# Optimization experiments

Hardware: AMD Instinct MI355X
Metric: run time of the kernel (lower is better)

The kernel has to match this reference:

```python
import jax, jax.numpy as jnp
import numpy as np

N, E, NG, H, BD, L, B = 4000, 50000, 12, 128, 128, 2, 100

def _gelu(x):
    return jax.nn.gelu(x, approximate=False)

def forward(pos, vel, charges, grid0, rand_SO3, batch, edge_index,
            W_basis1, b_basis1, W_basis2, b_basis2,
            W_fbasis1, b_fbasis1, W_fbasis2, b_fbasis2,
            W_embed, W_conv, W_fiber, b_conv, ln_gamma, ln_beta,
            W_ff1, b_ff1, W_ff2, b_ff2, W_ro1, b_ro1, W_ro2, b_ro2):
    n_nodes = pos.shape[0]
    n_graphs = rand_SO3.shape[0]
    n = grid0.shape[0]
    src, dst = edge_index[0], edge_index[1]
    # per-graph randomly rotated S2 grid
    grid_graph = jnp.einsum('bij,nj->bni', rand_SO3, grid0)    # [B,n,3]
    grid_node = grid_graph[batch]                               # [N,n,3]
    grid_edge = grid_node[src]                                  # [E,n,3]
    # R3S2 Euclidean invariants (separable): parallel + perpendicular parts of rel_pos wrt each grid orientation
    rel = pos[src] - pos[dst]                                   # [E,3]
    inv1 = jnp.einsum('ed,end->en', rel, grid_edge)[..., None]  # [E,n,1]
    inv2 = jnp.linalg.norm(rel[:, None, :] - inv1 * grid_edge, axis=-1, keepdims=True)
    cp = (charges[src] * charges[dst])[:, None, :]              # [E,1,1]
    ei = jnp.concatenate([inv1, inv2, jnp.broadcast_to(cp, inv1.shape)], -1)  # [E,n,3]
    # PolynomialFeatures(degree=2): [x, flatten(x outer x)] -> 3+9=12
    ei_poly = jnp.concatenate([ei, (ei[..., :, None] * ei[..., None, :]).reshape(ei.shape[:-1] + (9,))], -1)
    basis = _gelu(_gelu(ei_poly @ W_basis1 + b_basis1) @ W_basis2 + b_basis2)  # [E,n,BD]
    # fiber invariants: pairwise grid dot products (rotation cancels) -> [n,n,1]; poly deg 2 -> [n,n,2]
    fi = jnp.sum(grid0[:, None, :] * grid0[None, :, :], -1, keepdims=True)
    fi_poly = jnp.concatenate([fi, fi * fi], -1)
    fiber_basis = _gelu(_gelu(fi_poly @ W_fbasis1 + b_fbasis1) @ W_fbasis2 + b_fbasis2)  # [n,n,BD]
    # node features projected to sphere
    ones = jnp.ones((n_nodes, 1), pos.dtype)
    cnt = jax.ops.segment_sum(ones, batch, num_segments=n_graphs)
    mean_pos = jax.ops.segment_sum(pos, batch, num_segments=n_graphs) / jnp.maximum(cnt, 1.0)
    rel_pos = pos - mean_pos[batch]
    v_sph = jnp.einsum('nd,nkd->nk', vel, grid_node)[..., None]
    p_sph = jnp.einsum('nd,nkd->nk', rel_pos, grid_node)[..., None]
    c_sph = jnp.broadcast_to(charges[:, None, :], (n_nodes, n, 1))
    vn = jnp.linalg.norm(vel, axis=-1, keepdims=True)
    vn_sph = jnp.broadcast_to(vn[:, None, :], (n_nodes, n, 1))
    x = jnp.concatenate([v_sph, p_sph, c_sph, vn_sph], -1) @ W_embed  # [N,n,H]
    # SeparableBundleConvNext stack
    for l in range(W_conv.shape[0]):
        kern = basis @ W_conv[l]                                       # [E,n,H]
        x1 = jax.ops.segment_sum(x[src] * kern, dst, num_segments=n_nodes)  # depthwise spatial conv + scatter-add
        fk = fiber_basis @ W_fiber[l]                                  # [n,n,H]
        x2 = jnp.einsum('boc,poc->bpc', x1, fk) / n + b_conv[l]        # depthwise fiber conv
        mu = jnp.mean(x2, -1, keepdims=True)
        var = jnp.mean((x2 - mu) ** 2, -1, keepdims=True)
        h = (x2 - mu) / jnp.sqrt(var + 1e-5) * ln_gamma[l] + ln_beta[l]
        h = _gelu(h @ W_ff1[l] + b_ff1[l]) @ W_ff2[l] + b_ff2[l]
        x = x + h
    y = _gelu(x @ W_ro1 + b_ro1) @ W_ro2 + b_ro2                       # [N,n,1]
    return jnp.mean(grid_node * y, axis=-2)                            # sphere2vec -> [N,3]

def setup_inputs():
    key = jax.random.key(0)
    ks = jax.random.split(key, 24)
    f = jnp.float32
    # deterministic uniform-ish S2 grid (fibonacci sphere)
    i = np.arange(NG) + 0.5
    phi = np.arccos(1.0 - 2.0 * i / NG)
    th = np.pi * (1.0 + 5.0 ** 0.5) * i
    grid0 = jnp.asarray(np.stack([np.sin(phi) * np.cos(th), np.sin(phi) * np.sin(th), np.cos(phi)], -1), f)
    # random SO(3) per graph via unit quaternions
    q = jax.random.normal(ks[0], (B, 4), f)
    q = q / jnp.linalg.norm(q, axis=-1, keepdims=True)
    w, xq, yq, zq = q[:, 0], q[:, 1], q[:, 2], q[:, 3]
    R = jnp.stack([
        jnp.stack([1 - 2 * (yq ** 2 + zq ** 2), 2 * (xq * yq - zq * w), 2 * (xq * zq + yq * w)], -1),
        jnp.stack([2 * (xq * yq + zq * w), 1 - 2 * (xq ** 2 + zq ** 2), 2 * (yq * zq - xq * w)], -1),
        jnp.stack([2 * (xq * zq - yq * w), 2 * (yq * zq + xq * w), 1 - 2 * (xq ** 2 + yq ** 2)], -1)], -2)
    s = 0.05
    return dict(
        pos=jax.random.normal(ks[1], (N, 3), f),
        vel=jax.random.normal(ks[2], (N, 3), f),
        charges=jax.random.normal(ks[3], (N, 1), f),
        batch=jnp.sort(jax.random.randint(ks[4], (N,), 0, B)),
        edge_index=jax.random.randint(ks[5], (2, E), 0, N),
        grid0=grid0, rand_SO3=R,
        W_basis1=jax.random.normal(ks[6], (12, H), f) * s, b_basis1=jnp.zeros((H,), f),
        W_basis2=jax.random.normal(ks[7], (H, BD), f) * s, b_basis2=jnp.zeros((BD,), f),
        W_fbasis1=jax.random.normal(ks[8], (2, H), f) * s, b_fbasis1=jnp.zeros((H,), f),
        W_fbasis2=jax.random.normal(ks[9], (H, BD), f) * s, b_fbasis2=jnp.zeros((BD,), f),
        W_embed=jax.random.normal(ks[10], (4, H), f) * s,
        W_conv=jax.random.normal(ks[11], (L, BD, H), f) * s,
        W_fiber=jax.random.normal(ks[12], (L, BD, H), f) * s,
        b_conv=jnp.zeros((L, H), f),
        ln_gamma=jnp.ones((L, H), f), ln_beta=jnp.zeros((L, H), f),
        W_ff1=jax.random.normal(ks[13], (L, H, 4 * H), f) * s, b_ff1=jnp.zeros((L, 4 * H), f),
        W_ff2=jax.random.normal(ks[14], (L, 4 * H, H), f) * s, b_ff2=jnp.zeros((L, H), f),
        W_ro1=jax.random.normal(ks[15], (H, H), f) * s, b_ro1=jnp.zeros((H,), f),
        W_ro2=jax.random.normal(ks[16], (H, 1), f) * s, b_ro2=jnp.zeros((1,), f),
    )

def reference(pos, vel, charges, batch, edge_index, grid0, rand_SO3,
              W_basis1, b_basis1, W_basis2, b_basis2,
              W_fbasis1, b_fbasis1, W_fbasis2, b_fbasis2,
              W_embed, W_conv, W_fiber, b_conv, ln_gamma, ln_beta,
              W_ff1, b_ff1, W_ff2, b_ff2, W_ro1, b_ro1, W_ro2, b_ro2):
    return forward(pos, vel, charges, grid0, rand_SO3, batch, edge_index,
                   W_basis1, b_basis1, W_basis2, b_basis2,
                   W_fbasis1, b_fbasis1, W_fbasis2, b_fbasis2,
                   W_embed, W_conv, W_fiber, b_conv, ln_gamma, ln_beta,
                   W_ff1, b_ff1, W_ff2, b_ff2, W_ro1, b_ro1, W_ro2, b_ro2)
```

## Files before the change

### kernel.cpp

```cpp
#include <hip/hip_runtime.h>

typedef unsigned short u16;
typedef short s16x8 __attribute__((ext_vector_type(8)));
typedef float f32x4 __attribute__((ext_vector_type(4)));

constexpr int NNODES = 4000;
constexpr int NEDGES = 50000;
constexpr int NGRID  = 12;
constexpr int HD     = 128;
constexpr int H4     = 512;
constexpr int NLAY   = 2;

constexpr size_t OFF_GN   = 0;
constexpr size_t OFF_PS   = 144000;
constexpr size_t OFF_CNT  = 144304;
constexpr size_t OFF_FK   = 144512;
constexpr size_t OFF_X    = 181376;
constexpr size_t OFF_X1   = 6325376;
constexpr size_t OFF_WB   = 12469376;
constexpr size_t OFF_ROWP = 12625024;
constexpr size_t OFF_DEG  = 12629032;
constexpr size_t OFF_CUR  = 12633032;
constexpr size_t OFF_ESRT = 12637032;
constexpr size_t OFF_EIPB = 12687032;
constexpr size_t OFF_W1T  = 17487416;
constexpr size_t OFF_SRCS = 17489464;
constexpr size_t OFF_END_SLOW = 17539464;
constexpr size_t OFF_BAS  = 17539464;
constexpr size_t KERN_F   = 38400000;
constexpr size_t OFF_END_FAST  = OFF_BAS + KERN_F;
constexpr size_t OFF_END_DUAL  = OFF_BAS + 2*KERN_F;

constexpr size_t WB_W2T = 0;
constexpr size_t WB_WCT = 16384;
constexpr size_t WB_F1T = 49152;
constexpr size_t WB_F2T = 180224;

__device__ __forceinline__ u16 f2bf(float f){
  union { float f; unsigned int i; } v; v.f = f;
  unsigned int x = v.i;
  x += 0x7fffu + ((x >> 16) & 1u);
  return (u16)(x >> 16);
}
__device__ __forceinline__ float bf2f(u16 u){
  union { unsigned int i; float f; } v; v.i = ((unsigned int)u) << 16; return v.f;
}
__device__ __forceinline__ float gelu_f(float x){
  return 0.5f * x * (1.0f + erff(x * 0.70710678118654752f));
}
__device__ __forceinline__ float waveReduceSum(float v){
  #pragma unroll
  for(int off = 32; off > 0; off >>= 1) v += __shfl_xor(v, off, 64);
  return v;
}
__device__ __forceinline__ f32x4 mfma16(s16x8 a, s16x8 b, f32x4 c){
  return __builtin_amdgcn_mfma_f32_16x16x32_bf16(a, b, c, 0, 0, 0);
}

__global__ void k_stats(const float* __restrict__ pos, const int* __restrict__ batch,
                        float* __restrict__ possum, float* __restrict__ pcnt){
  int n = blockIdx.x * 256 + threadIdx.x;
  if(n >= NNODES) return;
  int b = batch[n];
  atomicAdd(&possum[b*3+0], pos[n*3+0]);
  atomicAdd(&possum[b*3+1], pos[n*3+1]);
  atomicAdd(&possum[b*3+2], pos[n*3+2]);
  atomicAdd(&pcnt[b], 1.0f);
}

__global__ void k_gridnode(const float* __restrict__ g0, const float* __restrict__ R,
                           const int* __restrict__ batch, float* __restrict__ grid_node){
  int idx = blockIdx.x * 256 + threadIdx.x;
  if(idx >= NNODES*NGRID) return;
  int n = idx / NGRID, k = idx % NGRID;
  int b = batch[n];
  float g[3];
  #pragma unroll
  for(int j=0;j<3;j++) g[j] = g0[k*3+j];
  #pragma unroll
  for(int i=0;i<3;i++){
    float s = 0.f;
    #pragma unroll
    for(int j=0;j<3;j++) s += R[b*9+i*3+j] * g[j];
    grid_node[idx*3+i] = s;
  }
}

__global__ __launch_bounds__(128) void k_embed(
    const float* __restrict__ pos, const float* __restrict__ vel, const float* __restrict__ charges,
    const int* __restrict__ batch, const float* __restrict__ possum, const float* __restrict__ pcnt,
    const float* __restrict__ grid_node, const float* __restrict__ W_embed, float* __restrict__ x)
{
  int n = blockIdx.x; int t = threadIdx.x;
  __shared__ float feats[NGRID][4];
  __shared__ float sgn[NGRID][3];
  if(t < 36) sgn[t/3][t%3] = grid_node[n*36 + t];
  __syncthreads();
  if(t < NGRID){
    int b = batch[n];
    float inv = 1.0f / fmaxf(pcnt[b], 1.0f);
    float v0=vel[n*3], v1=vel[n*3+1], v2=vel[n*3+2];
    float p0=pos[n*3]   - possum[b*3]*inv;
    float p1=pos[n*3+1] - possum[b*3+1]*inv;
    float p2=pos[n*3+2] - possum[b*3+2]*inv;
    float g0=sgn[t][0], g1=sgn[t][1], g2=sgn[t][2];
    feats[t][0] = v0*g0 + v1*g1 + v2*g2;
    feats[t][1] = p0*g0 + p1*g1 + p2*g2;
    feats[t][2] = charges[n];
    feats[t][3] = sqrtf(v0*v0 + v1*v1 + v2*v2);
  }
  __syncthreads();
  float w0=W_embed[0*HD+t], w1=W_embed[1*HD+t];
  float w2=W_embed[2*HD+t], w3=W_embed[3*HD+t];
  #pragma unroll
  for(int k=0;k<NGRID;k++)
    x[(n*NGRID+k)*HD + t] = feats[k][0]*w0 + feats[k][1]*w1 + feats[k][2]*w2 + feats[k][3]*w3;
}

__global__ __launch_bounds__(128) void k_fiber(
    const float* __restrict__ g0, const float* __restrict__ Wf1, const float* __restrict__ bfb1,
    const float* __restrict__ Wf2, const float* __restrict__ bfb2, const float* __restrict__ W_fiber,
    float* __restrict__ fk)
{
  int po = blockIdx.x; int p = po / NGRID, o = po % NGRID; int c = threadIdx.x;
  __shared__ float st[HD];
  __shared__ float sfb[HD];
  float fi = 0.f;
  #pragma unroll
  for(int j=0;j<3;j++) fi += g0[p*3+j] * g0[o*3+j];
  float f2 = fi*fi;
  st[c] = gelu_f(fi*Wf1[c] + f2*Wf1[HD+c] + bfb1[c]);
  __syncthreads();
  float a = bfb2[c];
  for(int j=0;j<HD;j++) a += st[j] * Wf2[j*HD+c];
  sfb[c] = gelu_f(a);
  __syncthreads();
  for(int l=0;l<NLAY;l++){
    float s = 0.f;
    for(int j=0;j<HD;j++) s += sfb[j] * W_fiber[l*HD*HD + j*HD + c];
    fk[(l*144 + po)*HD + c] = s;
  }
}

__global__ void k_prep(const float* __restrict__ W_b2, const float* __restrict__ W_b1,
                       const float* __restrict__ W_conv, const float* __restrict__ W_ff1,
                       const float* __restrict__ W_ff2,
                       u16* __restrict__ W2T, u16* __restrict__ W1T, u16* __restrict__ WCT,
                       u16* __restrict__ F1T, u16* __restrict__ F2T){
  int idx = blockIdx.x * 256 + threadIdx.x;
  if(idx < 16384){
    int r = idx >> 7, c = idx & 127;
    W2T[c*128 + r] = f2bf(W_b2[idx]);
    return;
  }
  idx -= 16384;
  if(idx < 4096){
    int c = idx >> 5, f = idx & 31;
    W1T[idx] = (f < 12) ? f2bf(W_b1[f*HD + c]) : (u16)0;
    return;
  }
  idx -= 4096;
  if(idx < 32768){
    int l = idx >> 14, j = idx & 16383;
    int r = j >> 7, c = j & 127;
    WCT[l*16384 + c*128 + r] = f2bf(W_conv[l*16384 + j]);
    return;
  }
  idx -= 32768;
  if(idx < 131072){
    int l = idx >> 16, j = idx & 65535;
    int r = j / 512, c = j % 512;
    F1T[l*65536 + c*128 + r] = f2bf(W_ff1[l*65536 + j]);
    return;
  }
  idx -= 131072;
  if(idx < 131072){
    int l = idx >> 16, j = idx & 65535;
    int r = j / 128, c = j % 128;
    F2T[l*65536 + c*512 + r] = f2bf(W_ff2[l*65536 + j]);
  }
}

__global__ void k_prepro(const float* __restrict__ W_ro1, u16* __restrict__ RO1T){
  int idx = blockIdx.x * 256 + threadIdx.x;
  if(idx >= 16384) return;
  int r = idx >> 7, c = idx & 127;
  RO1T[c*128 + r] = f2bf(W_ro1[idx]);
}

__global__ void k_deg(const int* __restrict__ eidx, int* __restrict__ deg){
  int e = blockIdx.x * 256 + threadIdx.x;
  if(e >= NEDGES) return;
  atomicAdd(&deg[eidx[NEDGES + e]], 1);
}

__global__ __launch_bounds__(256) void k_scan(const int* __restrict__ deg, int* __restrict__ rowptr){
  int t = threadIdx.x;
  __shared__ int part[256];
  int base = t * 16;
  int lp[16]; int s = 0;
  #pragma unroll
  for(int i=0;i<16;i++){
    int idx = base + i;
    int v = (idx < NNODES) ? deg[idx] : 0;
    lp[i] = s; s += v;
  }
  part[t] = s;
  __syncthreads();
  for(int off=1; off<256; off<<=1){
    int v2 = (t >= off) ? part[t-off] : 0;
    __syncthreads();
    part[t] += v2;
    __syncthreads();
  }
  int excl = part[t] - s;
  #pragma unroll
  for(int i=0;i<16;i++){
    int idx = base + i;
    if(idx < NNODES) rowptr[idx] = excl + lp[i];
  }
  if(t == 255) rowptr[NNODES] = part[255];
}

__global__ void k_bucket(const int* __restrict__ eidx, const int* __restrict__ rowptr,
                         int* __restrict__ cur, int* __restrict__ esorted, int* __restrict__ srcs){
  int e = blockIdx.x * 256 + threadIdx.x;
  if(e >= NEDGES) return;
  int d = eidx[NEDGES + e];
  int p = atomicAdd(&cur[d], 1);
  int slot = rowptr[d] + p;
  esorted[slot] = e;
  srcs[slot] = eidx[e];
}

__global__ void k_einv(const int* __restrict__ esorted, const int* __restrict__ eidx,
                       const float* __restrict__ pos, const float* __restrict__ charges,
                       const float* __restrict__ grid_node, u16* __restrict__ eipb){
  int row = blockIdx.x * 256 + threadIdx.x;
  if(row >= NEDGES*NGRID) return;
  int p = row / NGRID, kg = row - p*NGRID;
  int e = esorted[p];
  int sr = eidx[e], ds = eidx[NEDGES + e];
  float r0 = pos[sr*3]   - pos[ds*3];
  float r1 = pos[sr*3+1] - pos[ds*3+1];
  float r2 = pos[sr*3+2] - pos[ds*3+2];
  float cp = charges[sr] * charges[ds];
  float g0 = grid_node[sr*36 + kg*3];
  float g1 = grid_node[sr*36 + kg*3 + 1];
  float g2 = grid_node[sr*36 + kg*3 + 2];
  float inv1 = r0*g0 + r1*g1 + r2*g2;
  float d0 = r0 - inv1*g0, d1 = r1 - inv1*g1, d2 = r2 - inv1*g2;
  float inv2 = sqrtf(d0*d0 + d1*d1 + d2*d2);
  float ei[3] = {inv1, inv2, cp};
  s16x8 lo, hi;
  #pragma unroll
  for(int i=0;i<3;i++) lo[i] = (short)f2bf(ei[i]);
  lo[3] = (short)f2bf(ei[0]*ei[0]);
  lo[4] = (short)f2bf(ei[0]*ei[1]);
  lo[5] = (short)f2bf(ei[0]*ei[2]);
  lo[6] = (short)f2bf(ei[1]*ei[0]);
  lo[7] = (short)f2bf(ei[1]*ei[1]);
  hi[0] = (short)f2bf(ei[1]*ei[2]);
  hi[1] = (short)f2bf(ei[2]*ei[0]);
  hi[2] = (short)f2bf(ei[2]*ei[1]);
  hi[3] = (short)f2bf(ei[2]*ei[2]);
  hi[4] = 0; hi[5] = 0; hi[6] = 0; hi[7] = 0;
  *(s16x8*)&eipb[(size_t)row*16]     = lo;
  *(s16x8*)&eipb[(size_t)row*16 + 8] = hi;
}

constexpr int T1S = 136;

__global__ __launch_bounds__(256) void k_kern(
    const u16* __restrict__ eipb, const u16* __restrict__ W1T,
    const float* __restrict__ b1, const float* __restrict__ b2,
    const u16* __restrict__ W2T, const u16* __restrict__ WCT,
    u16* __restrict__ kern, int nl, size_t kstride)
{
  int t = threadIdx.x;
  int lane = t & 63, w = t >> 6, quad = lane >> 4, l16 = lane & 15;
  size_t R0 = (size_t)blockIdx.x * 64;
  __shared__ __align__(16) u16 s_buf[64*T1S];

  float b1v[2], b2v[2];
  #pragma unroll
  for(int nt=0;nt<2;nt++){
    b1v[nt] = b1[(2*w+nt)*16 + l16];
    b2v[nt] = b2[(2*w+nt)*16 + l16];
  }
  const s16x8 zvec = {0,0,0,0,0,0,0,0};

  {
    f32x4 a1[4][2];
    #pragma unroll
    for(int mt=0;mt<4;mt++)
      #pragma unroll
      for(int nt=0;nt<2;nt++) a1[mt][nt] = (f32x4){0.f,0.f,0.f,0.f};
    s16x8 Af[4];
    #pragma unroll
    for(int mt=0;mt<4;mt++){
      s16x8 v = *(const s16x8*)&eipb[(R0 + mt*16 + l16)*16 + (quad&1)*8];
      if(quad >= 2) v = zvec;
      Af[mt] = v;
    }
    #pragma unroll
    for(int nt=0;nt<2;nt++){
      s16x8 Bf = *(const s16x8*)&W1T[((2*w+nt)*16 + l16)*32 + quad*8];
      #pragma unroll
      for(int mt=0;mt<4;mt++) a1[mt][nt] = mfma16(Af[mt], Bf, a1[mt][nt]);
    }
    #pragma unroll
    for(int mt=0;mt<4;mt++)
      #pragma unroll
      for(int nt=0;nt<2;nt++)
        #pragma unroll
        for(int i=0;i<4;i++)
          s_buf[(mt*16 + quad*4 + i)*T1S + (2*w+nt)*16 + l16] = f2bf(gelu_f(a1[mt][nt][i] + b1v[nt]));
  }
  __syncthreads();
  f32x4 a2[4][2];
  #pragma unroll
  for(int mt=0;mt<4;mt++)
    #pragma unroll
    for(int nt=0;nt<2;nt++) a2[mt][nt] = (f32x4){0.f,0.f,0.f,0.f};
  #pragma unroll
  for(int ks=0; ks<4; ks++){
    s16x8 Af[4];
    #pragma unroll
    for(int mt=0;mt<4;mt++)
      Af[mt] = *(const s16x8*)&s_buf[(mt*16 + l16)*T1S + ks*32 + quad*8];
    #pragma unroll
    for(int nt=0;nt<2;nt++){
      s16x8 Bf = *(const s16x8*)&W2T[((2*w+nt)*16 + l16)*HD + ks*32 + quad*8];
      #pragma unroll
      for(int mt=0;mt<4;mt++) a2[mt][nt] = mfma16(Af[mt], Bf, a2[mt][nt]);
    }
  }
  __syncthreads();
  #pragma unroll
  for(int mt=0;mt<4;mt++)
    #pragma unroll
    for(int nt=0;nt<2;nt++)
      #pragma unroll
      for(int i=0;i<4;i++)
        s_buf[(mt*16 + quad*4 + i)*T1S + (2*w+nt)*16 + l16] = f2bf(gelu_f(a2[mt][nt][i] + b2v[nt]));
  __syncthreads();
  for(int l=0; l<nl; l++){
    f32x4 a3[4][2];
    #pragma unroll
    for(int mt=0;mt<4;mt++)
      #pragma unroll
      for(int nt=0;nt<2;nt++) a3[mt][nt] = (f32x4){0.f,0.f,0.f,0.f};
    #pragma unroll
    for(int ks=0; ks<4; ks++){
      s16x8 Af[4];
      #pragma unroll
      for(int mt=0;mt<4;mt++)
        Af[mt] = *(const s16x8*)&s_buf[(mt*16 + l16)*T1S + ks*32 + quad*8];
      #pragma unroll
      for(int nt=0;nt<2;nt++){
        s16x8 Bf = *(const s16x8*)&WCT[l*16384 + ((2*w+nt)*16 + l16)*HD + ks*32 + quad*8];
        #pragma unroll
        for(int mt=0;mt<4;mt++) a3[mt][nt] = mfma16(Af[mt], Bf, a3[mt][nt]);
      }
    }
    #pragma unroll
    for(int mt=0;mt<4;mt++)
      #pragma unroll
      for(int nt=0;nt<2;nt++)
        #pragma unroll
        for(int i=0;i<4;i++)
          kern[l*kstride + (R0 + mt*16 + quad*4 + i)*HD + (2*w+nt)*16 + l16] = f2bf(a3[mt][nt][i]);
  }
}

__global__ __launch_bounds__(256) void k_gather(
    const u16* __restrict__ kern, const float* __restrict__ x,
    const int* __restrict__ rowptr, const int* __restrict__ srcs,
    const float* __restrict__ fkl, const float* __restrict__ bconv,
    const float* __restrict__ gamma, const float* __restrict__ beta,
    u16* __restrict__ hout)
{
  int n = blockIdx.x, t = threadIdx.x;
  int c = t & 127, half = t >> 7;
  int w = t >> 6, lane = t & 63;
  __shared__ float raw[NGRID*HD];
  __shared__ float red[4][6], red2[4][6];
  int base = rowptr[n];
  int d = rowptr[n+1] - base;
  float acc[6] = {0.f,0.f,0.f,0.f,0.f,0.f};
  int srcn = (d > 0) ? srcs[base] : 0;
  for(int e=0; e<d; e++){
    int nsrc = (e+1 < d) ? srcs[base+e+1] : 0;
    const u16*   kp = &kern[((size_t)(base+e)*NGRID + half*6)*HD + c];
    const float* xp = &x[((size_t)srcn*NGRID + half*6)*HD + c];
    #pragma unroll
    for(int kk=0;kk<6;kk++)
      acc[kk] += bf2f(kp[kk*HD]) * xp[kk*HD];
    srcn = nsrc;
  }
  #pragma unroll
  for(int kk=0;kk<6;kk++)
    raw[(half*6+kk)*HD + c] = acc[kk];
  __syncthreads();
  float bc = bconv[c];
  float v[6];
  #pragma unroll
  for(int kk=0;kk<6;kk++){
    int p = half*6 + kk;
    float a = 0.f;
    #pragma unroll
    for(int o=0;o<NGRID;o++)
      a += raw[o*HD + c] * fkl[(p*NGRID+o)*HD + c];
    v[kk] = a * (1.0f/12.0f) + bc;
  }
  #pragma unroll
  for(int kk=0;kk<6;kk++){
    float s = waveReduceSum(v[kk]);
    if(lane == 0) red[w][kk] = s;
  }
  __syncthreads();
  float dd[6];
  #pragma unroll
  for(int kk=0;kk<6;kk++){
    float mu = (red[half*2][kk] + red[half*2+1][kk]) * (1.0f/128.0f);
    dd[kk] = v[kk] - mu;
    float s2 = waveReduceSum(dd[kk]*dd[kk]);
    if(lane == 0) red2[w][kk] = s2;
  }
  __syncthreads();
  float ga = gamma[c], be = beta[c];
  #pragma unroll
  for(int kk=0;kk<6;kk++){
    float var = (red2[half*2][kk] + red2[half*2+1][kk]) * (1.0f/128.0f);
    float inv = 1.0f / sqrtf(var + 1e-5f);
    hout[((size_t)n*NGRID + half*6 + kk)*HD + c] = f2bf(dd[kk] * inv * ga + be);
  }
}

__global__ __launch_bounds__(256) void k_ff1(
    const u16* __restrict__ F1T, const float* __restrict__ bf1,
    const u16* __restrict__ hin, u16* __restrict__ h4)
{
  int t = threadIdx.x;
  size_t r0 = (size_t)blockIdx.x * 32;
  int lane = t & 63, w = t >> 6, quad = lane >> 4, l16 = lane & 15;
  __shared__ __align__(16) u16 sxh[32*T1S];
  for(int i=t; i<32*HD/8; i+=256){
    int r = (i*8) >> 7, cc = (i*8) & 127;
    *(s16x8*)&sxh[r*T1S + cc] = *(const s16x8*)&hin[r0*HD + (size_t)i*8];
  }
  __syncthreads();
  f32x4 acc[2][8];
  #pragma unroll
  for(int mt=0;mt<2;mt++)
    #pragma unroll
    for(int j=0;j<8;j++) acc[mt][j] = (f32x4){0.f,0.f,0.f,0.f};
  #pragma unroll
  for(int ks=0; ks<4; ks++){
    s16x8 Af0 = *(const s16x8*)&sxh[l16*T1S + ks*32 + quad*8];
    s16x8 Af1 = *(const s16x8*)&sxh[(16 + l16)*T1S + ks*32 + quad*8];
    #pragma unroll
    for(int j=0;j<8;j++){
      int nt = w*8 + j;
      s16x8 Bf = *(const s16x8*)&F1T[((size_t)(nt*16 + l16))*HD + ks*32 + quad*8];
      acc[0][j] = mfma16(Af0, Bf, acc[0][j]);
      acc[1][j] = mfma16(Af1, Bf, acc[1][j]);
    }
  }
  #pragma unroll
  for(int j=0;j<8;j++){
    int col = (w*8+j)*16 + l16;
    float bv = bf1[col];
    #pragma unroll
    for(int mt=0;mt<2;mt++)
      #pragma unroll
      for(int i=0;i<4;i++){
        int row = mt*16 + quad*4 + i;
        h4[(r0 + row)*H4 + col] = f2bf(gelu_f(acc[mt][j][i] + bv));
      }
  }
}

__global__ __launch_bounds__(256) void k_ff2(
    const u16* __restrict__ F2T, const float* __restrict__ bf2,
    const u16* __restrict__ h4, float* __restrict__ x)
{
  int t = threadIdx.x;
  size_t r0 = (size_t)blockIdx.x * 32;
  int lane = t & 63, w = t >> 6, quad = lane >> 4, l16 = lane & 15;
  f32x4 acc[2][2];
  #pragma unroll
  for(int mt=0;mt<2;mt++)
    #pragma unroll
    for(int j=0;j<2;j++) acc[mt][j] = (f32x4){0.f,0.f,0.f,0.f};
  for(int ks=0; ks<16; ks++){
    s16x8 Af0 = *(const s16x8*)&h4[(r0 + l16)*H4 + ks*32 + quad*8];
    s16x8 Af1 = *(const s16x8*)&h4[(r0 + 16 + l16)*H4 + ks*32 + quad*8];
    #pragma unroll
    for(int j=0;j<2;j++){
      int nt = w*2 + j;
      s16x8 Bf = *(const s16x8*)&F2T[((size_t)(nt*16 + l16))*H4 + ks*32 + quad*8];
      acc[0][j] = mfma16(Af0, Bf, acc[0][j]);
      acc[1][j] = mfma16(Af1, Bf, acc[1][j]);
    }
  }
  #pragma unroll
  for(int j=0;j<2;j++){
    int col = (w*2+j)*16 + l16;
    float bv = bf2[col];
    #pragma unroll
    for(int mt=0;mt<2;mt++)
      #pragma unroll
      for(int i=0;i<4;i++){
        size_t row = r0 + mt*16 + quad*4 + i;
        x[row*HD + col] += acc[mt][j][i] + bv;
      }
  }
}

__global__ __launch_bounds__(256) void k_conv_slow(
    const u16* __restrict__ eipb, const u16* __restrict__ W1T,
    const float* __restrict__ b1, const float* __restrict__ b2,
    const u16* __restrict__ W2T, const u16* __restrict__ WCT,
    const float* __restrict__ x,
    const int* __restrict__ rowptr, const int* __restrict__ srcs,
    float* __restrict__ x1o)
{
  int n = blockIdx.x; int t = threadIdx.x;
  int lane = t & 63, w = t >> 6, quad = lane >> 4, l16 = lane & 15;

  __shared__ __align__(16) u16 s_t1h[48*T1S];
  __shared__ __align__(16) u16 s_bas[48*T1S];
  __shared__ __align__(16) float accLDS[NGRID*HD];

  int base = rowptr[n];
  int d = rowptr[n+1] - base;

  float b1v[2], b2v[2];
  #pragma unroll
  for(int nt=0;nt<2;nt++){
    b1v[nt] = b1[(2*w+nt)*16 + l16];
    b2v[nt] = b2[(2*w+nt)*16 + l16];
  }

  for(int i=t; i<NGRID*HD; i+=256) accLDS[i] = 0.f;
  __syncthreads();

  f32x4 accv[3][2];
  #pragma unroll
  for(int mt=0;mt<3;mt++)
    #pragma unroll
    for(int nt=0;nt<2;nt++) accv[mt][nt] = (f32x4){0.f,0.f,0.f,0.f};

  const s16x8 zvec = {0,0,0,0,0,0,0,0};

  for(int ch=0; ch<d; ch+=4){
    size_t rowb = (size_t)(base + ch) * NGRID;
    s16x8 Af1[3];
    #pragma unroll
    for(int mt=0;mt<3;mt++){
      s16x8 v = *(const s16x8*)&eipb[(rowb + mt*16 + l16)*16 + (quad&1)*8];
      if(quad >= 2) v = zvec;
      Af1[mt] = v;
    }
    float xv[3][4][2];
    #pragma unroll
    for(int mt=0;mt<3;mt++)
      #pragma unroll
      for(int i=0;i<4;i++){
        int row = mt*16 + quad*4 + i;
        int e = row / 12;
        int k = row - e*12;
        int ei2 = base + ch + e;
        int srcn = srcs[min(ei2, NEDGES-1)];
        float m = (ch + e < d) ? 1.0f : 0.0f;
        const float* xp = &x[((size_t)srcn*NGRID + k)*HD + l16];
        #pragma unroll
        for(int nt=0;nt<2;nt++)
          xv[mt][i][nt] = xp[(2*w+nt)*16] * m;
      }
    {
      f32x4 a1[3][2];
      #pragma unroll
      for(int mt=0;mt<3;mt++)
        #pragma unroll
        for(int nt=0;nt<2;nt++) a1[mt][nt] = (f32x4){0.f,0.f,0.f,0.f};
      #pragma unroll
      for(int nt=0;nt<2;nt++){
        s16x8 Bf = *(const s16x8*)&W1T[((2*w+nt)*16 + l16)*32 + quad*8];
        #pragma unroll
        for(int mt=0;mt<3;mt++) a1[mt][nt] = mfma16(Af1[mt], Bf, a1[mt][nt]);
      }
      #pragma unroll
      for(int mt=0;mt<3;mt++)
        #pragma unroll
        for(int nt=0;nt<2;nt++)
          #pragma unroll
          for(int i=0;i<4;i++)
            s_t1h[(mt*16 + quad*4 + i)*T1S + (2*w+nt)*16 + l16] = f2bf(gelu_f(a1[mt][nt][i] + b1v[nt]));
    }
    __syncthreads();
    {
      f32x4 a2[3][2];
      #pragma unroll
      for(int mt=0;mt<3;mt++)
        #pragma unroll
        for(int nt=0;nt<2;nt++) a2[mt][nt] = (f32x4){0.f,0.f,0.f,0.f};
      #pragma unroll
      for(int ks=0; ks<4; ks++){
        s16x8 Af[3];
        #pragma unroll
        for(int mt=0;mt<3;mt++)
          Af[mt] = *(const s16x8*)&s_t1h[(mt*16 + l16)*T1S + ks*32 + quad*8];
        #pragma unroll
        for(int nt=0;nt<2;nt++){
          s16x8 Bf = *(const s16x8*)&W2T[((2*w+nt)*16 + l16)*HD + ks*32 + quad*8];
          #pragma unroll
          for(int mt=0;mt<3;mt++) a2[mt][nt] = mfma16(Af[mt], Bf, a2[mt][nt]);
        }
      }
      #pragma unroll
      for(int mt=0;mt<3;mt++)
        #pragma unroll
        for(int nt=0;nt<2;nt++)
          #pragma unroll
          for(int i=0;i<4;i++)
            s_bas[(mt*16 + quad*4 + i)*T1S + (2*w+nt)*16 + l16] = f2bf(gelu_f(a2[mt][nt][i] + b2v[nt]));
    }
    __syncthreads();
    {
      f32x4 a3[3][2];
      #pragma unroll
      for(int mt=0;mt<3;mt++)
        #pragma unroll
        for(int nt=0;nt<2;nt++) a3[mt][nt] = (f32x4){0.f,0.f,0.f,0.f};
      #pragma unroll
      for(int ks=0; ks<4; ks++){
        s16x8 Af[3];
        #pragma unroll
        for(int mt=0;mt<3;mt++)
          Af[mt] = *(const s16x8*)&s_bas[(mt*16 + l16)*T1S + ks*32 + quad*8];
        #pragma unroll
        for(int nt=0;nt<2;nt++){
          s16x8 Bf = *(const s16x8*)&WCT[((2*w+nt)*16 + l16)*HD + ks*32 + quad*8];
          #pragma unroll
          for(int mt=0;mt<3;mt++) a3[mt][nt] = mfma16(Af[mt], Bf, a3[mt][nt]);
        }
      }
      #pragma unroll
      for(int mt=0;mt<3;mt++)
        #pragma unroll
        for(int nt=0;nt<2;nt++)
          #pragma unroll
          for(int i=0;i<4;i++)
            accv[mt][nt][i] += a3[mt][nt][i] * xv[mt][i][nt];
    }
  }
  __syncthreads();
  #pragma unroll
  for(int mt=0;mt<3;mt++)
    #pragma unroll
    for(int nt=0;nt<2;nt++)
      #pragma unroll
      for(int i=0;i<4;i++){
        int row = mt*16 + quad*4 + i;
        int k = row % 12;
        atomicAdd(&accLDS[k*HD + (2*w+nt)*16 + l16], accv[mt][nt][i]);
      }
  __syncthreads();
  for(int i=t; i<NGRID*HD; i+=256)
    x1o[(size_t)n*NGRID*HD + i] = accLDS[i];
}

constexpr int STS = 520;
__global__ __launch_bounds__(256) void k_ffln(
    const u16* __restrict__ F1T, const float* __restrict__ bf1,
    const u16* __restrict__ F2T, const float* __restrict__ bf2,
    const float* __restrict__ x1raw,
    const float* __restrict__ fkl, const float* __restrict__ bconv,
    const float* __restrict__ gamma, const float* __restrict__ beta,
    float* __restrict__ x)
{
  int n = blockIdx.x; int t = threadIdx.x;
  int lane = t & 63, w = t >> 6, quad = lane >> 4, l16 = lane & 15;
  __shared__ __align__(16) float raw[NGRID*HD];
  __shared__ __align__(16) u16 sxh[16*T1S];
  __shared__ __align__(16) u16 st[16*STS];

  for(int i=t; i<NGRID*HD; i+=256) raw[i] = x1raw[(size_t)n*NGRID*HD + i];
  for(int i=t; i<4*T1S; i+=256) sxh[12*T1S + i] = 0;
  __syncthreads();

  {
    int c0 = lane, c1 = lane + 64;
    float bc0 = bconv[c0], bc1 = bconv[c1];
    float ga0 = gamma[c0], ga1 = gamma[c1];
    float be0 = beta[c0],  be1 = beta[c1];
    #pragma unroll
    for(int pp=0; pp<3; pp++){
      int p = w + pp*4;
      float a0 = 0.f, a1 = 0.f;
      #pragma unroll
      for(int o=0;o<NGRID;o++){
        a0 += raw[o*HD + c0] * fkl[(p*NGRID+o)*HD + c0];
        a1 += raw[o*HD + c1] * fkl[(p*NGRID+o)*HD + c1];
      }
      float v0 = a0 * (1.0f/12.0f) + bc0;
      float v1 = a1 * (1.0f/12.0f) + bc1;
      float mu = waveReduceSum(v0 + v1) * (1.0f/128.0f);
      float d0 = v0 - mu, d1 = v1 - mu;
      float var = waveReduceSum(d0*d0 + d1*d1) * (1.0f/128.0f);
      float inv = 1.0f / sqrtf(var + 1e-5f);
      sxh[p*T1S + c0] = f2bf(d0 * inv * ga0 + be0);
      sxh[p*T1S + c1] = f2bf(d1 * inv * ga1 + be1);
    }
  }
  __syncthreads();
  {
    f32x4 acc1[8];
    #pragma unroll
    for(int j=0;j<8;j++) acc1[j] = (f32x4){0.f,0.f,0.f,0.f};
    #pragma unroll
    for(int ks=0; ks<4; ks++){
      s16x8 Af = *(const s16x8*)&sxh[l16*T1S + ks*32 + quad*8];
      #pragma unroll
      for(int j=0;j<8;j++){
        int nt = w*8 + j;
        s16x8 Bf = *(const s16x8*)&F1T[((size_t)(nt*16 + l16))*HD + ks*32 + quad*8];
        acc1[j] = mfma16(Af, Bf, acc1[j]);
      }
    }
    #pragma unroll
    for(int j=0;j<8;j++){
      int col = (w*8+j)*16 + l16;
      float bv = bf1[col];
      #pragma unroll
      for(int i=0;i<4;i++){
        int row = quad*4 + i;
        st[row*STS + col] = f2bf(gelu_f(acc1[j][i] + bv));
      }
    }
  }
  __syncthreads();
  {
    f32x4 acc2[2];
    #pragma unroll
    for(int j=0;j<2;j++) acc2[j] = (f32x4){0.f,0.f,0.f,0.f};
    for(int ks=0; ks<16; ks++){
      s16x8 Af = *(const s16x8*)&st[l16*STS + ks*32 + quad*8];
      #pragma unroll
      for(int j=0;j<2;j++){
        int nt = w*2 + j;
        s16x8 Bf = *(const s16x8*)&F2T[((size_t)(nt*16 + l16))*H4 + ks*32 + quad*8];
        acc2[j] = mfma16(Af, Bf, acc2[j]);
      }
    }
    #pragma unroll
    for(int j=0;j<2;j++){
      int col = (w*2+j)*16 + l16;
      float bv = bf2[col];
      #pragma unroll
      for(int i=0;i<4;i++){
        int row = quad*4 + i;
        if(row < NGRID){
          size_t idx = ((size_t)n*NGRID + row)*HD + col;
          x[idx] += acc2[j][i] + bv;
        }
      }
    }
  }
}

__global__ __launch_bounds__(256) void k_readout(
    const float* __restrict__ x, const float* __restrict__ grid_node,
    const u16* __restrict__ RO1T, const float* __restrict__ br1,
    const float* __restrict__ Wr2, const float* __restrict__ br2,
    float* __restrict__ out)
{
  int t = threadIdx.x;
  int n0 = blockIdx.x * 2;
  int lane = t & 63, w = t >> 6, quad = lane >> 4, l16 = lane & 15;
  __shared__ __align__(16) u16 sxh[32*T1S];
  __shared__ float sy[32];
  if(t < 32) sy[t] = 0.f;
  for(int i=t; i<2*NGRID*HD; i+=256){
    int nd = i / (NGRID*HD), rem = i - nd*NGRID*HD;
    int r = rem >> 7, c = rem & 127;
    sxh[(nd*16 + r)*T1S + c] = f2bf(x[(size_t)n0*NGRID*HD + i]);
  }
  for(int i=t; i<4*T1S; i+=256){ sxh[12*T1S + i] = 0; sxh[28*T1S + i] = 0; }
  __syncthreads();
  f32x4 acc[2][2];
  #pragma unroll
  for(int mt=0;mt<2;mt++)
    #pragma unroll
    for(int j=0;j<2;j++) acc[mt][j] = (f32x4){0.f,0.f,0.f,0.f};
  #pragma unroll
  for(int ks=0; ks<4; ks++){
    s16x8 Af0 = *(const s16x8*)&sxh[l16*T1S + ks*32 + quad*8];
    s16x8 Af1 = *(const s16x8*)&sxh[(16 + l16)*T1S + ks*32 + quad*8];
    #pragma unroll
    for(int j=0;j<2;j++){
      int nt = w*2 + j;
      s16x8 Bf = *(const s16x8*)&RO1T[((size_t)(nt*16 + l16))*HD + ks*32 + quad*8];
      acc[0][j] = mfma16(Af0, Bf, acc[0][j]);
      acc[1][j] = mfma16(Af1, Bf, acc[1][j]);
    }
  }
  #pragma unroll
  for(int j=0;j<2;j++){
    int col = (w*2+j)*16 + l16;
    float bv = br1[col];
    float w2v = Wr2[col];
    #pragma unroll
    for(int mt=0;mt<2;mt++)
      #pragma unroll
      for(int i=0;i<4;i++){
        int row = quad*4 + i;
        if(row < NGRID)
          atomicAdd(&sy[mt*16 + row], gelu_f(acc[mt][j][i] + bv) * w2v);
      }
  }
  __syncthreads();
  if(t < 6){
    int nd = t / 3, d = t - nd*3;
    float b2v = br2[0];
    float s = 0.f;
    #pragma unroll
    for(int k=0;k<NGRID;k++)
      s += grid_node[((size_t)(n0+nd)*NGRID + k)*3 + d] * (sy[nd*16 + k] + b2v);
    out[(n0+nd)*3 + d] = s * (1.0f/12.0f);
  }
}

extern "C" void kernel_launch(void* const* d_in, const int* in_sizes, int n_in,
                              void* d_out, int out_size, void* d_ws, size_t ws_size,
                              hipStream_t stream)
{
  const float* pos      = (const float*)d_in[0];
  const float* vel      = (const float*)d_in[1];
  const float* charges  = (const float*)d_in[2];
  const int*   batch    = (const int*)d_in[3];
  const int*   eidx     = (const int*)d_in[4];
  const float* grid0    = (const float*)d_in[5];
  const float* R        = (const float*)d_in[6];
  const float* W_b1     = (const float*)d_in[7];
  const float* b_b1     = (const float*)d_in[8];
  const float* W_b2     = (const float*)d_in[9];
  const float* b_b2     = (const float*)d_in[10];
  const float* W_fb1    = (const float*)d_in[11];
  const float* b_fb1    = (const float*)d_in[12];
  const float* W_fb2    = (const float*)d_in[13];
  const float* b_fb2    = (const float*)d_in[14];
  const float* W_embed  = (const float*)d_in[15];
  const float* W_conv   = (const float*)d_in[16];
  const float* W_fiber  = (const float*)d_in[17];
  const float* b_conv   = (const float*)d_in[18];
  const float* ln_g     = (const float*)d_in[19];
  const float* ln_b     = (const float*)d_in[20];
  const float* W_ff1    = (const float*)d_in[21];
  const float* b_ff1    = (const float*)d_in[22];
  const float* W_ff2    = (const float*)d_in[23];
  const float* b_ff2    = (const float*)d_in[24];
  const float* W_ro1    = (const float*)d_in[25];
  const float* b_ro1    = (const float*)d_in[26];
  const float* W_ro2    = (const float*)d_in[27];
  const float* b_ro2    = (const float*)d_in[28];

  float* ws        = (float*)d_ws;
  float* grid_node = ws + OFF_GN;
  float* possum    = ws + OFF_PS;
  float* pcnt      = ws + OFF_CNT;
  float* fk        = ws + OFF_FK;
  float* x         = ws + OFF_X;
  float* x1        = ws + OFF_X1;
  u16*   WB        = (u16*)(ws + OFF_WB);
  u16*   W2T       = WB + WB_W2T;
  u16*   WCT       = WB + WB_WCT;
  u16*   F1T       = WB + WB_F1T;
  u16*   F2T       = WB + WB_F2T;
  int*   rowptr    = (int*)(ws + OFF_ROWP);
  int*   deg       = (int*)(ws + OFF_DEG);
  int*   cur       = (int*)(ws + OFF_CUR);
  int*   esorted   = (int*)(ws + OFF_ESRT);
  u16*   eipb      = (u16*)(ws + OFF_EIPB);
  u16*   W1T       = (u16*)(ws + OFF_W1T);
  int*   srcs      = (int*)(ws + OFF_SRCS);
  u16*   kern1     = (u16*)(ws + OFF_BAS);
  u16*   RO1T      = (u16*)(ws + OFF_ESRT);
  u16*   hbuf      = (u16*)x1;
  const size_t KSTR = (size_t)600000 * HD;

  const bool fast = (ws_size >= OFF_END_FAST * sizeof(float));
  const bool dual = (ws_size >= OFF_END_DUAL * sizeof(float));

  hipMemsetAsync(possum, 0, 512*sizeof(float), stream);
  hipMemsetAsync(deg, 0, NNODES*sizeof(int), stream);
  hipMemsetAsync(cur, 0, NNODES*sizeof(int), stream);
  hipMemsetAsync(eipb + (size_t)NEDGES*NGRID*16, 0, 48*16*sizeof(u16), stream);

  k_stats<<<(NNODES+255)/256, 256, 0, stream>>>(pos, batch, possum, pcnt);
  k_gridnode<<<(NNODES*NGRID+255)/256, 256, 0, stream>>>(grid0, R, batch, grid_node);
  k_embed<<<NNODES, 128, 0, stream>>>(pos, vel, charges, batch, possum, pcnt, grid_node, W_embed, x);
  k_fiber<<<144, 128, 0, stream>>>(grid0, W_fb1, b_fb1, W_fb2, b_fb2, W_fiber, fk);

  k_prep<<<(315392+255)/256, 256, 0, stream>>>(W_b2, W_b1, W_conv, W_ff1, W_ff2,
                                               W2T, W1T, WCT, F1T, F2T);

  k_deg<<<(NEDGES+255)/256, 256, 0, stream>>>(eidx, deg);
  k_scan<<<1, 256, 0, stream>>>(deg, rowptr);
  k_bucket<<<(NEDGES+255)/256, 256, 0, stream>>>(eidx, rowptr, cur, esorted, srcs);

  k_einv<<<(NEDGES*NGRID+255)/256, 256, 0, stream>>>(esorted, eidx, pos, charges, grid_node, eipb);
  k_prepro<<<64, 256, 0, stream>>>(W_ro1, RO1T);

  if(fast){
    if(dual)
      k_kern<<<9375, 256, 0, stream>>>(eipb, W1T, b_b1, b_b2, W2T, WCT, kern1, 2, KSTR);
    for(int l=0; l<NLAY; l++){
      if(!dual)
        k_kern<<<9375, 256, 0, stream>>>(eipb, W1T, b_b1, b_b2, W2T, WCT + (size_t)l*16384,
                                         kern1, 1, 0);
      const u16* kl = dual ? (kern1 + (size_t)l*KSTR) : kern1;
      u16* h4 = dual ? (kern1 + (size_t)l*KSTR) : kern1;
      k_gather<<<NNODES, 256, 0, stream>>>(kl, x, rowptr, srcs,
          fk + (size_t)l*144*HD, b_conv + l*HD, ln_g + l*HD, ln_b + l*HD, hbuf);
      k_ff1<<<NNODES*NGRID/32, 256, 0, stream>>>(F1T + (size_t)l*65536, b_ff1 + l*H4, hbuf, h4);
      k_ff2<<<NNODES*NGRID/32, 256, 0, stream>>>(F2T + (size_t)l*65536, b_ff2 + l*HD, h4, x);
    }
  } else {
    for(int l=0; l<NLAY; l++){
      k_conv_slow<<<NNODES, 256, 0, stream>>>(eipb, W1T, b_b1, b_b2, W2T, WCT + (size_t)l*16384,
          x, rowptr, srcs, x1);
      k_ffln<<<NNODES, 256, 0, stream>>>(F1T + (size_t)l*65536, b_ff1 + l*H4,
          F2T + (size_t)l*65536, b_ff2 + l*HD, x1,
          fk + (size_t)l*144*HD, b_conv + l*HD, ln_g + l*HD, ln_b + l*HD, x);
    }
  }

  k_readout<<<NNODES/2, 256, 0, stream>>>(x, grid_node, RO1T, b_ro1, W_ro2, b_ro2, (float*)d_out);
}
```

Before: 799.9 us.

## Process two nodes per block in gather with paired-channel vector loads and per-wave LayerNorm

The gather kernel now handles two destination nodes per 256-thread block, with each thread accumulating two adjacent channels through 32-bit bf16 and float2 loads. The per-grid-point LayerNorm is remapped so one wave owns a whole 128-channel row, which replaces the shared-memory cross-wave reductions and two of the barriers with plain wave reductions. This aims to cut memory instruction count and synchronisation in the edge gather. Per-node parallelism in the gather phase is halved. Two adjacent memsets (deg and cur) are merged into one call, which assumes the two buffers are contiguous in the workspace.

```diff
diff --git a/kernel.cpp b/kernel.cpp
--- a/kernel.cpp
+++ b/kernel.cpp
@@ -381,60 +381,68 @@
     const float* __restrict__ gamma, const float* __restrict__ beta,
     u16* __restrict__ hout)
 {
-  int n = blockIdx.x, t = threadIdx.x;
-  int c = t & 127, half = t >> 7;
-  int w = t >> 6, lane = t & 63;
-  __shared__ float raw[NGRID*HD];
-  __shared__ float red[4][6], red2[4][6];
-  int base = rowptr[n];
-  int d = rowptr[n+1] - base;
-  float acc[6] = {0.f,0.f,0.f,0.f,0.f,0.f};
-  int srcn = (d > 0) ? srcs[base] : 0;
-  for(int e=0; e<d; e++){
-    int nsrc = (e+1 < d) ? srcs[base+e+1] : 0;
-    const u16*   kp = &kern[((size_t)(base+e)*NGRID + half*6)*HD + c];
-    const float* xp = &x[((size_t)srcn*NGRID + half*6)*HD + c];
+  int t = threadIdx.x;
+  __shared__ float raw[2][NGRID*HD];
+  {
+    int nd = t >> 7;
+    int tt = t & 127;
+    int g  = tt >> 6;
+    int c2 = (tt & 63) * 2;
+    int n = blockIdx.x * 2 + nd;
+    int base = rowptr[n];
+    int d = rowptr[n+1] - base;
+    float2 acc[6];
+    #pragma unroll
+    for(int kk=0;kk<6;kk++){ acc[kk].x = 0.f; acc[kk].y = 0.f; }
+    int srcn = (d > 0) ? srcs[base] : 0;
+    for(int e=0; e<d; e++){
+      int nsrc = (e+1 < d) ? srcs[base+e+1] : 0;
+      const u16*   kp = &kern[((size_t)(base+e)*NGRID + g*6)*HD + c2];
+      const float* xp = &x[((size_t)srcn*NGRID + g*6)*HD + c2];
+      #pragma unroll
+      for(int kk=0;kk<6;kk++){
+        unsigned int u = *(const unsigned int*)(kp + kk*HD);
+        float2 xv = *(const float2*)(xp + kk*HD);
+        acc[kk].x += bf2f((u16)(u & 0xffffu)) * xv.x;
+        acc[kk].y += bf2f((u16)(u >> 16))     * xv.y;
+      }
+      srcn = nsrc;
+    }
     #pragma unroll
     for(int kk=0;kk<6;kk++)
-      acc[kk] += bf2f(kp[kk*HD]) * xp[kk*HD];
-    srcn = nsrc;
-  }
-  #pragma unroll
-  for(int kk=0;kk<6;kk++)
-    raw[(half*6+kk)*HD + c] = acc[kk];
-  __syncthreads();
-  float bc = bconv[c];
-  float v[6];
-  #pragma unroll
-  for(int kk=0;kk<6;kk++){
-    int p = half*6 + kk;
-    float a = 0.f;
-    #pragma unroll
-    for(int o=0;o<NGRID;o++)
-      a += raw[o*HD + c] * fkl[(p*NGRID+o)*HD + c];
-    v[kk] = a * (1.0f/12.0f) + bc;
-  }
-  #pragma unroll
-  for(int kk=0;kk<6;kk++){
-    float s = waveReduceSum(v[kk]);
-    if(lane == 0) red[w][kk] = s;
-  }
-  __syncthreads();
-  float dd[6];
-  #pragma unroll
-  for(int kk=0;kk<6;kk++){
-    float mu = (red[half*2][kk] + red[half*2+1][kk]) * (1.0f/128.0f);
-    dd[kk] = v[kk] - mu;
-    float s2 = waveReduceSum(dd[kk]*dd[kk]);
-    if(lane == 0) red2[w][kk] = s2;
-  }
-  __syncthreads();
-  float ga = gamma[c], be = beta[c];
-  #pragma unroll
-  for(int kk=0;kk<6;kk++){
-    float var = (red2[half*2][kk] + red2[half*2+1][kk]) * (1.0f/128.0f);
-    float inv = 1.0f / sqrtf(var + 1e-5f);
-    hout[((size_t)n*NGRID + half*6 + kk)*HD + c] = f2bf(dd[kk] * inv * ga + be);
+      *(float2*)&raw[nd][(g*6+kk)*HD + c2] = acc[kk];
+  }
+  __syncthreads();
+  {
+    int w = t >> 6, lane = t & 63;
+    int ndw = w >> 1, ph = w & 1;
+    int c2 = lane * 2;
+    int nn = blockIdx.x * 2 + ndw;
+    float2 bc = *(const float2*)&bconv[c2];
+    float2 ga = *(const float2*)&gamma[c2];
+    float2 be = *(const float2*)&beta[c2];
+    #pragma unroll
+    for(int kk=0;kk<6;kk++){
+      int p = ph*6 + kk;
+      float ax = 0.f, ay = 0.f;
+      #pragma unroll
+      for(int o=0;o<NGRID;o++){
+        float2 fv = *(const float2*)&fkl[(p*NGRID+o)*HD + c2];
+        float2 rv = *(const float2*)&raw[ndw][o*HD + c2];
+        ax += rv.x * fv.x;
+        ay += rv.y * fv.y;
+      }
+      float vx = ax * (1.0f/12.0f) + bc.x;
+      float vy = ay * (1.0f/12.0f) + bc.y;
+      float mu = waveReduceSum(vx + vy) * (1.0f/128.0f);
+      float dx = vx - mu, dy = vy - mu;
+      float var = waveReduceSum(dx*dx + dy*dy) * (1.0f/128.0f);
+      float inv = 1.0f / sqrtf(var + 1e-5f);
+      u16 h0 = f2bf(dx * inv * ga.x + be.x);
+      u16 h1 = f2bf(dy * inv * ga.y + be.y);
+      unsigned int pu = (unsigned int)h0 | ((unsigned int)h1 << 16);
+      *(unsigned int*)&hout[((size_t)nn*NGRID + p)*HD + c2] = pu;
+    }
   }
 }
 
@@ -896,8 +904,7 @@
   const bool dual = (ws_size >= OFF_END_DUAL * sizeof(float));
 
   hipMemsetAsync(possum, 0, 512*sizeof(float), stream);
-  hipMemsetAsync(deg, 0, NNODES*sizeof(int), stream);
-  hipMemsetAsync(cur, 0, NNODES*sizeof(int), stream);
+  hipMemsetAsync(deg, 0, 2*NNODES*sizeof(int), stream);
   hipMemsetAsync(eipb + (size_t)NEDGES*NGRID*16, 0, 48*16*sizeof(u16), stream);
 
   k_stats<<<(NNODES+255)/256, 256, 0, stream>>>(pos, batch, possum, pcnt);
@@ -924,7 +931,7 @@
                                          kern1, 1, 0);
       const u16* kl = dual ? (kern1 + (size_t)l*KSTR) : kern1;
       u16* h4 = dual ? (kern1 + (size_t)l*KSTR) : kern1;
-      k_gather<<<NNODES, 256, 0, stream>>>(kl, x, rowptr, srcs,
+      k_gather<<<NNODES/2, 256, 0, stream>>>(kl, x, rowptr, srcs,
           fk + (size_t)l*144*HD, b_conv + l*HD, ln_g + l*HD, ln_b + l*HD, hbuf);
       k_ff1<<<NNODES*NGRID/32, 256, 0, stream>>>(F1T + (size_t)l*65536, b_ff1 + l*H4, hbuf, h4);
       k_ff2<<<NNODES*NGRID/32, 256, 0, stream>>>(F2T + (size_t)l*65536, b_ff2 + l*HD, h4, x);
```

Measured after the change: 823.3 us. 1.03x slower.
